# Performance work log

Hardware: AMD Instinct MI355X
Metric: run time of the kernel (lower is better)

Reference implementation:

```python
import jax, jax.numpy as jnp
import numpy as np

N_NODES = 50000
N_EDGES = 800000
D_IN = 128
D_OUT = 128


def setup_inputs() -> dict:
    key = jax.random.key(0)
    k_x, k_r, k_c, k_v, k_w = jax.random.split(key, 5)
    x = jax.random.normal(k_x, (N_NODES, D_IN), dtype=jnp.float32)
    edge_row = jax.random.randint(k_r, (N_EDGES,), 0, N_NODES)  # destination nodes
    edge_col = jax.random.randint(k_c, (N_EDGES,), 0, N_NODES)  # source nodes
    edge_val = jax.random.uniform(k_v, (N_EDGES,), dtype=jnp.float32)
    W = jax.random.normal(k_w, (D_OUT, D_IN), dtype=jnp.float32) * (1.0 / np.sqrt(D_IN))
    bias = jnp.zeros((D_OUT,), dtype=jnp.float32)
    return {"x": x, "edge_row": edge_row, "edge_col": edge_col,
            "edge_val": edge_val, "W": W, "bias": bias}


def reference(x, edge_row, edge_col, edge_val, W, bias):
    # support = linear(x)   (nn.Linear with bias=False: x @ W.T)
    support = jnp.einsum('ni,oi->no', x, W)  # [N, D_OUT]
    # out = sparse.mm(adj, support): gather source rows, scale by edge value,
    # scatter-add into destination rows.
    msgs = edge_val[:, None] * support[edge_col]  # [E, D_OUT]
    out = jax.ops.segment_sum(msgs, edge_row, num_segments=N_NODES)
    return out + bias
```

## Files before the change

kernel.cpp:

```cpp
#include <hip/hip_runtime.h>
#include <hip/hip_bf16.h>


constexpr int D     = 128;
constexpr int NPB   = 64;
constexpr int CAP   = 2048;
constexpr int C1    = 3200;
constexpr int BT    = 1024;
constexpr int NBMAX = 1024;

__device__ inline unsigned int bf1(float f) {
    unsigned int u = __float_as_uint(f);
    return (u + 0x7fffu + ((u >> 16) & 1u)) >> 16;
}
__device__ inline unsigned int bf2(float lo, float hi) {
    return bf1(lo) | (bf1(hi) << 16);
}
__device__ inline float bflo(unsigned int u) { return __uint_as_float(u << 16); }
__device__ inline float bfhi(unsigned int u) { return __uint_as_float(u & 0xffff0000u); }

__global__ __launch_bounds__(256) void cvt_bf16_kernel(const float* __restrict__ in,
                                                       uint4* __restrict__ out, int n8,
                                                       int* __restrict__ gcursor, int nb) {
    int i = blockIdx.x * 256 + threadIdx.x;
    if (i < nb) gcursor[i] = 0;
    if (i >= n8) return;
    const float4* p = (const float4*)in + (size_t)i * 2;
    float4 a = p[0], b = p[1];
    uint4 r;
    r.x = bf2(a.x, a.y); r.y = bf2(a.z, a.w);
    r.z = bf2(b.x, b.y); r.w = bf2(b.z, b.w);
    out[i] = r;
}

__global__ __launch_bounds__(256) void gemm_mfma_kernel(const float* __restrict__ x,
                                                        const unsigned short* __restrict__ Wb,
                                                        unsigned short* __restrict__ supb,
                                                        int n_nodes) {
    using frag  = __attribute__((ext_vector_type(8))) short;
    using f32x4 = __attribute__((ext_vector_type(4))) float;
    const int wv = threadIdx.x >> 6;
    const int lane = threadIdx.x & 63;
    const int m = lane & 15, quad = lane >> 4;
    const int row0 = blockIdx.x * 64 + wv * 16;
    const int rowc = min(row0 + m, n_nodes - 1);

    frag a[4];
#pragma unroll
    for (int kf = 0; kf < 4; ++kf) {
        const float4* xp = (const float4*)(x + (size_t)rowc * D + kf * 32 + quad * 8);
        float4 p = xp[0], q = xp[1];
        frag t;
        t[0] = (short)bf1(p.x); t[1] = (short)bf1(p.y);
        t[2] = (short)bf1(p.z); t[3] = (short)bf1(p.w);
        t[4] = (short)bf1(q.x); t[5] = (short)bf1(q.y);
        t[6] = (short)bf1(q.z); t[7] = (short)bf1(q.w);
        a[kf] = t;
    }

    f32x4 acc[8];
#pragma unroll
    for (int ct = 0; ct < 8; ++ct) acc[ct] = (f32x4){0.f, 0.f, 0.f, 0.f};

#pragma unroll
    for (int ct = 0; ct < 8; ++ct) {
        const unsigned short* wrow = Wb + (size_t)(ct * 16 + m) * D;
#pragma unroll
        for (int kf = 0; kf < 4; ++kf) {
            frag b = *(const frag*)(wrow + kf * 32 + quad * 8);
            acc[ct] = __builtin_amdgcn_mfma_f32_16x16x32_bf16(a[kf], b, acc[ct], 0, 0, 0);
        }
    }

#pragma unroll
    for (int ct = 0; ct < 8; ++ct) {
#pragma unroll
        for (int r = 0; r < 4; ++r) {
            int rr = row0 + quad * 4 + r;
            if (rr < n_nodes)
                supb[(size_t)rr * D + ct * 16 + m] = (unsigned short)bf1(acc[ct][r]);
        }
    }
}

__global__ __launch_bounds__(BT) void binpass_kernel(const int* __restrict__ erow,
                                                     const int* __restrict__ ecol,
                                                     const float* __restrict__ eval,
                                                     int* __restrict__ gcursor,
                                                     int2* __restrict__ coarse,
                                                     int n_edges, int nb) {
    __shared__ int bkcnt[NBMAX];
    __shared__ int bkoff[NBMAX];
    __shared__ int sscan[BT];
    __shared__ int gbase[NBMAX];
    __shared__ unsigned short slotbk[C1];
    __shared__ int2 stage[C1];
    const int t = threadIdx.x;
    const int base = blockIdx.x * C1;
    const int m = min(C1, n_edges - base);

    for (int i = t; i < nb; i += BT) bkcnt[i] = 0;
    __syncthreads();

    constexpr int EPT = (C1 + BT - 1) / BT;
    int  bk[EPT], rank[EPT];
    int2 pk[EPT];
#pragma unroll
    for (int j = 0; j < EPT; ++j) {
        int i = t + j * BT;
        bk[j] = -1;
        if (i < m) {
            int e = base + i;
            int dst = erow[e];
            int b = dst / NPB;
            bk[j] = b;
            rank[j] = atomicAdd(&bkcnt[b], 1);
            pk[j] = make_int2(ecol[e] | ((dst & (NPB - 1)) << 20),
                              __float_as_int(eval[e]));
        }
    }
    __syncthreads();

    {
        int v = (t < nb) ? bkcnt[t] : 0;
        sscan[t] = v;
        __syncthreads();
        for (int o = 1; o < BT; o <<= 1) {
            int u = (t >= o) ? sscan[t - o] : 0;
            __syncthreads();
            sscan[t] += u;
            __syncthreads();
        }
        if (t < nb) bkoff[t] = sscan[t] - v;
    }
    __syncthreads();

#pragma unroll
    for (int j = 0; j < EPT; ++j) {
        if (bk[j] >= 0) {
            int s = bkoff[bk[j]] + rank[j];
            stage[s] = pk[j];
            slotbk[s] = (unsigned short)bk[j];
        }
    }
    if (t < nb) {
        int c = bkcnt[t];
        gbase[t] = (c > 0) ? (t * CAP + atomicAdd(&gcursor[t], c)) : 0;
    }
    __syncthreads();

    for (int i = t; i < m; i += BT) {
        int b = slotbk[i];
        int p = gbase[b] + (i - bkoff[b]);
        if (p < (b + 1) * CAP) coarse[p] = stage[i];
    }
}

__global__ __launch_bounds__(BT) void sortgather_kernel(const int* __restrict__ gcursor,
                                                        const int2* __restrict__ coarse,
                                                        const unsigned short* __restrict__ supb,
                                                        const float* __restrict__ bias,
                                                        float* __restrict__ out,
                                                        int n_nodes) {
    __shared__ int ncnt[NPB];
    __shared__ int noff[NPB];
    __shared__ int ncur[NPB];
    __shared__ int2 sorted[CAP];
    const int t = threadIdx.x;
    const int b = blockIdx.x;
    const int node0 = b * NPB;
    const int m = min(gcursor[b], CAP);
    const int2* src = coarse + (size_t)b * CAP;

    if (t < NPB) ncnt[t] = 0;
    __syncthreads();

    for (int i = t; i < m; i += BT)
        atomicAdd(&ncnt[(src[i].x >> 20) & (NPB - 1)], 1);
    __syncthreads();

    if (t < NPB) {
        int v = ncnt[t];
        int inc = v;
        for (int o = 1; o < NPB; o <<= 1) {
            int u = __shfl_up(inc, o, 64);
            if (t >= o) inc += u;
        }
        noff[t] = inc - v;
        ncur[t] = inc - v;
    }
    __syncthreads();

    for (int i = t; i < m; i += BT) {
        int2 e = src[i];
        int dl = (e.x >> 20) & (NPB - 1);
        int p = atomicAdd(&ncur[dl], 1);
        sorted[p] = make_int2(e.x & 0xFFFFF, e.y);
    }
    __syncthreads();

    const int qw = t >> 4;
    const int l16 = t & 15;
    const int node = node0 + qw;
    if (node >= n_nodes) return;
    const int beg = noff[qw];
    const int end = beg + ncnt[qw];

    const float4* b4 = (const float4*)(bias + l16 * 8);
    float4 acc0 = b4[0], acc1 = b4[1];

    int e = beg;
    for (; e + 1 < end; e += 2) {
        int2 d0 = sorted[e], d1 = sorted[e + 1];
        uint4 u0 = *(const uint4*)(supb + (size_t)d0.x * D + l16 * 8);
        uint4 u1 = *(const uint4*)(supb + (size_t)d1.x * D + l16 * 8);
        float v0 = __int_as_float(d0.y), v1 = __int_as_float(d1.y);
        acc0.x += v0 * bflo(u0.x) + v1 * bflo(u1.x);
        acc0.y += v0 * bfhi(u0.x) + v1 * bfhi(u1.x);
        acc0.z += v0 * bflo(u0.y) + v1 * bflo(u1.y);
        acc0.w += v0 * bfhi(u0.y) + v1 * bfhi(u1.y);
        acc1.x += v0 * bflo(u0.z) + v1 * bflo(u1.z);
        acc1.y += v0 * bfhi(u0.z) + v1 * bfhi(u1.z);
        acc1.z += v0 * bflo(u0.w) + v1 * bflo(u1.w);
        acc1.w += v0 * bfhi(u0.w) + v1 * bfhi(u1.w);
    }
    if (e < end) {
        int2 d0 = sorted[e];
        uint4 u0 = *(const uint4*)(supb + (size_t)d0.x * D + l16 * 8);
        float v0 = __int_as_float(d0.y);
        acc0.x += v0 * bflo(u0.x); acc0.y += v0 * bfhi(u0.x);
        acc0.z += v0 * bflo(u0.y); acc0.w += v0 * bfhi(u0.y);
        acc1.x += v0 * bflo(u0.z); acc1.y += v0 * bfhi(u0.z);
        acc1.z += v0 * bflo(u0.w); acc1.w += v0 * bfhi(u0.w);
    }
    float4* o4 = (float4*)(out + (size_t)node * D + l16 * 8);
    o4[0] = acc0;
    o4[1] = acc1;
}

__global__ __launch_bounds__(256) void init_out_kernel(float4* __restrict__ out4,
                                                       const float4* __restrict__ bias4,
                                                       int total4) {
    int i = blockIdx.x * 256 + threadIdx.x;
    if (i < total4) out4[i] = bias4[i & 31];
}

__global__ __launch_bounds__(256) void scatter_fb_kernel(const int* __restrict__ erow,
                                                         const int* __restrict__ ecol,
                                                         const float* __restrict__ eval,
                                                         const unsigned short* __restrict__ supb,
                                                         float* __restrict__ out,
                                                         int n_edges) {
    int e = blockIdx.x * 8 + (threadIdx.x >> 5);
    if (e >= n_edges) return;
    int lane = threadIdx.x & 31;
    int src = ecol[e], dst = erow[e];
    float v = eval[e];
    const unsigned short* sp = supb + (size_t)src * D + lane * 4;
    float* op = out + (size_t)dst * D + lane * 4;
#pragma unroll
    for (int j = 0; j < 4; ++j)
        atomicAdd(op + j, v * __uint_as_float(((unsigned)sp[j]) << 16));
}

static inline size_t align_up(size_t v, size_t a) { return (v + a - 1) & ~(a - 1); }

extern "C" void kernel_launch(void* const* d_in, const int* in_sizes, int n_in,
                              void* d_out, int out_size, void* d_ws, size_t ws_size,
                              hipStream_t stream) {
    const float* x    = (const float*)d_in[0];
    const int*   erow = (const int*)d_in[1];
    const int*   ecol = (const int*)d_in[2];
    const float* eval = (const float*)d_in[3];
    const float* W    = (const float*)d_in[4];
    const float* bias = (const float*)d_in[5];
    float* out = (float*)d_out;

    const int n_nodes = in_sizes[0] / D;
    const int n_edges = in_sizes[1];
    const int nb = (n_nodes + NPB - 1) / NPB;

    char* base = (char*)d_ws;
    size_t off = 0;
    unsigned short* supb = (unsigned short*)(base + off); off = align_up(off + (size_t)n_nodes * D * 2, 256);
    unsigned short* Wb   = (unsigned short*)(base + off); off = align_up(off + (size_t)D * D * 2, 256);
    int*  gcursor = (int*)(base + off);  off = align_up(off + (size_t)nb * 4, 256);
    int2* coarse  = (int2*)(base + off); off = align_up(off + (size_t)nb * CAP * 8, 256);

    const int n8 = D * D / 8;
    const int cvt_grid = (max(n8, nb) + 255) / 256;
    const bool fast = (n_nodes < (1 << 20)) && (nb <= NBMAX) && (off <= ws_size);

    cvt_bf16_kernel<<<cvt_grid, 256, 0, stream>>>(W, (uint4*)Wb, n8, gcursor, fast ? nb : 0);
    gemm_mfma_kernel<<<(n_nodes + 63) / 64, 256, 0, stream>>>(x, Wb, supb, n_nodes);

    if (fast) {
        binpass_kernel<<<(n_edges + C1 - 1) / C1, BT, 0, stream>>>(
            erow, ecol, eval, gcursor, coarse, n_edges, nb);
        sortgather_kernel<<<nb, BT, 0, stream>>>(
            gcursor, coarse, supb, bias, out, n_nodes);
    } else {
        int total4 = n_nodes * (D / 4);
        init_out_kernel<<<(total4 + 255) / 256, 256, 0, stream>>>(
            (float4*)out, (const float4*)bias, total4);
        scatter_fb_kernel<<<(n_edges + 7) / 8, 256, 0, stream>>>(
            erow, ecol, eval, supb, out, n_edges);
    }
}
```

Measured before the change: 148.3 us.

## Double GEMM rows per wave, use hardware bf16 convert, shuffle-based bin scan

Each GEMM wave now computes two 16-row tiles, so every W fragment it loads is reused for twice as many MFMAs, and the grid is halved to match. The hand-rolled bf16 rounding for x and W is replaced by the packed __float22bfloat162_rn intrinsic. The binpass prefix scan drops its 10-step shared-memory loop, which had two barriers per step, in favour of a wave-level __shfl_up scan followed by a small scan over the 16 per-wave sums. The costs are higher register pressure in the GEMM and fewer blocks in flight.

```diff
diff --git a/kernel.cpp b/kernel.cpp
--- a/kernel.cpp
+++ b/kernel.cpp
@@ -15,6 +15,10 @@
 }
 __device__ inline unsigned int bf2(float lo, float hi) {
     return bf1(lo) | (bf1(hi) << 16);
+}
+__device__ inline unsigned int cvt2(float a, float b) {
+    __hip_bfloat162 h = __float22bfloat162_rn(float2{a, b});
+    return *reinterpret_cast<unsigned int*>(&h);
 }
 __device__ inline float bflo(unsigned int u) { return __uint_as_float(u << 16); }
 __device__ inline float bfhi(unsigned int u) { return __uint_as_float(u & 0xffff0000u); }
@@ -28,8 +32,8 @@
     const float4* p = (const float4*)in + (size_t)i * 2;
     float4 a = p[0], b = p[1];
     uint4 r;
-    r.x = bf2(a.x, a.y); r.y = bf2(a.z, a.w);
-    r.z = bf2(b.x, b.y); r.w = bf2(b.z, b.w);
+    r.x = cvt2(a.x, a.y); r.y = cvt2(a.z, a.w);
+    r.z = cvt2(b.x, b.y); r.w = cvt2(b.z, b.w);
     out[i] = r;
 }
 
@@ -39,28 +43,36 @@
                                                         int n_nodes) {
     using frag  = __attribute__((ext_vector_type(8))) short;
     using f32x4 = __attribute__((ext_vector_type(4))) float;
+    union FU { uint4 u; frag f; };
     const int wv = threadIdx.x >> 6;
     const int lane = threadIdx.x & 63;
     const int m = lane & 15, quad = lane >> 4;
-    const int row0 = blockIdx.x * 64 + wv * 16;
-    const int rowc = min(row0 + m, n_nodes - 1);
-
-    frag a[4];
+    const int row0 = blockIdx.x * 128 + wv * 32;
+    const int r0 = min(row0 + m, n_nodes - 1);
+    const int r1 = min(row0 + 16 + m, n_nodes - 1);
+
+    frag a0[4], a1[4];
 #pragma unroll
     for (int kf = 0; kf < 4; ++kf) {
-        const float4* xp = (const float4*)(x + (size_t)rowc * D + kf * 32 + quad * 8);
-        float4 p = xp[0], q = xp[1];
-        frag t;
-        t[0] = (short)bf1(p.x); t[1] = (short)bf1(p.y);
-        t[2] = (short)bf1(p.z); t[3] = (short)bf1(p.w);
-        t[4] = (short)bf1(q.x); t[5] = (short)bf1(q.y);
-        t[6] = (short)bf1(q.z); t[7] = (short)bf1(q.w);
-        a[kf] = t;
-    }
-
-    f32x4 acc[8];
-#pragma unroll
-    for (int ct = 0; ct < 8; ++ct) acc[ct] = (f32x4){0.f, 0.f, 0.f, 0.f};
+        const float4* xp0 = (const float4*)(x + (size_t)r0 * D + kf * 32 + quad * 8);
+        float4 p = xp0[0], q = xp0[1];
+        FU t;
+        t.u.x = cvt2(p.x, p.y); t.u.y = cvt2(p.z, p.w);
+        t.u.z = cvt2(q.x, q.y); t.u.w = cvt2(q.z, q.w);
+        a0[kf] = t.f;
+        const float4* xp1 = (const float4*)(x + (size_t)r1 * D + kf * 32 + quad * 8);
+        p = xp1[0]; q = xp1[1];
+        t.u.x = cvt2(p.x, p.y); t.u.y = cvt2(p.z, p.w);
+        t.u.z = cvt2(q.x, q.y); t.u.w = cvt2(q.z, q.w);
+        a1[kf] = t.f;
+    }
+
+    f32x4 acc0[8], acc1[8];
+#pragma unroll
+    for (int ct = 0; ct < 8; ++ct) {
+        acc0[ct] = (f32x4){0.f, 0.f, 0.f, 0.f};
+        acc1[ct] = (f32x4){0.f, 0.f, 0.f, 0.f};
+    }
 
 #pragma unroll
     for (int ct = 0; ct < 8; ++ct) {
@@ -68,7 +80,8 @@
 #pragma unroll
         for (int kf = 0; kf < 4; ++kf) {
             frag b = *(const frag*)(wrow + kf * 32 + quad * 8);
-            acc[ct] = __builtin_amdgcn_mfma_f32_16x16x32_bf16(a[kf], b, acc[ct], 0, 0, 0);
+            acc0[ct] = __builtin_amdgcn_mfma_f32_16x16x32_bf16(a0[kf], b, acc0[ct], 0, 0, 0);
+            acc1[ct] = __builtin_amdgcn_mfma_f32_16x16x32_bf16(a1[kf], b, acc1[ct], 0, 0, 0);
         }
     }
 
@@ -76,9 +89,12 @@
     for (int ct = 0; ct < 8; ++ct) {
 #pragma unroll
         for (int r = 0; r < 4; ++r) {
-            int rr = row0 + quad * 4 + r;
-            if (rr < n_nodes)
-                supb[(size_t)rr * D + ct * 16 + m] = (unsigned short)bf1(acc[ct][r]);
+            int rr0 = row0 + quad * 4 + r;
+            if (rr0 < n_nodes)
+                supb[(size_t)rr0 * D + ct * 16 + m] = (unsigned short)bf1(acc0[ct][r]);
+            int rr1 = row0 + 16 + quad * 4 + r;
+            if (rr1 < n_nodes)
+                supb[(size_t)rr1 * D + ct * 16 + m] = (unsigned short)bf1(acc1[ct][r]);
         }
     }
 }
@@ -91,7 +107,7 @@
                                                      int n_edges, int nb) {
     __shared__ int bkcnt[NBMAX];
     __shared__ int bkoff[NBMAX];
-    __shared__ int sscan[BT];
+    __shared__ int wsum[16];
     __shared__ int gbase[NBMAX];
     __shared__ unsigned short slotbk[C1];
     __shared__ int2 stage[C1];
@@ -122,16 +138,28 @@
     __syncthreads();
 
     {
+        const int w = t >> 6, l = t & 63;
         int v = (t < nb) ? bkcnt[t] : 0;
-        sscan[t] = v;
+        int inc = v;
+#pragma unroll
+        for (int o = 1; o < 64; o <<= 1) {
+            int u = __shfl_up(inc, o, 64);
+            if (l >= o) inc += u;
+        }
+        if (l == 63) wsum[w] = inc;
         __syncthreads();
-        for (int o = 1; o < BT; o <<= 1) {
-            int u = (t >= o) ? sscan[t - o] : 0;
-            __syncthreads();
-            sscan[t] += u;
-            __syncthreads();
-        }
-        if (t < nb) bkoff[t] = sscan[t] - v;
+        if (t < 16) {
+            int wv2 = wsum[t];
+            int winc = wv2;
+#pragma unroll
+            for (int o = 1; o < 16; o <<= 1) {
+                int u = __shfl_up(winc, o, 16);
+                if (t >= o) winc += u;
+            }
+            wsum[t] = winc - wv2;
+        }
+        __syncthreads();
+        if (t < nb) bkoff[t] = inc - v + wsum[w];
     }
     __syncthreads();
 
@@ -292,7 +320,7 @@
     const bool fast = (n_nodes < (1 << 20)) && (nb <= NBMAX) && (off <= ws_size);
 
     cvt_bf16_kernel<<<cvt_grid, 256, 0, stream>>>(W, (uint4*)Wb, n8, gcursor, fast ? nb : 0);
-    gemm_mfma_kernel<<<(n_nodes + 63) / 64, 256, 0, stream>>>(x, Wb, supb, n_nodes);
+    gemm_mfma_kernel<<<(n_nodes + 127) / 128, 256, 0, stream>>>(x, Wb, supb, n_nodes);
 
     if (fast) {
         binpass_kernel<<<(n_edges + C1 - 1) / C1, BT, 0, stream>>>(
```

Result: faster. 142.3 us (-4.1%).
